# Optimization experiments

Hardware: AMD Instinct MI355X
Metric: run time of the kernel (lower is better)

Reference implementation:

```python
import jax, jax.numpy as jnp
import numpy as np

ATTN_MASK_VALUE = -1e10
N = 8192
DIM = 1024
DIM_HEAD = 64
DIM_OUT = 1024

def setup_inputs() -> dict:
    key = jax.random.key(0)
    k1, k2, k3 = jax.random.split(key, 3)
    x = jax.random.normal(k1, (N, DIM), dtype=jnp.float32)
    Wqkv = jax.random.normal(k2, (DIM, 3 * DIM_HEAD), dtype=jnp.float32) * (DIM ** -0.5)
    Wout = jax.random.normal(k3, (DIM_HEAD, DIM_OUT), dtype=jnp.float32) * (DIM_HEAD ** -0.5)
    bout = jnp.zeros((DIM_OUT,), dtype=jnp.float32)
    return {"x": x, "Wqkv": Wqkv, "Wout": Wout, "bout": bout}

def reference(x, Wqkv, Wout, bout) -> jnp.ndarray:
    n = x.shape[0]
    scale = DIM_HEAD ** -0.5
    qkv = x @ Wqkv                      # [n, 3*dh]
    q, k, v = jnp.split(qkv, 3, axis=-1)  # each [n, dh]
    sim = jnp.einsum('id,jd->ij', q, k) * scale  # [n, n]
    mask = jnp.tril(jnp.ones((n, n), dtype=bool))
    sim = jnp.where(mask, sim, ATTN_MASK_VALUE)
    attn = jax.nn.softmax(sim, axis=-1)
    out = jnp.einsum('ij,jd->id', attn, v)  # [n, dh]
    return out @ Wout + bout            # [n, dim_out]
```

## Files before the change

kernel.cpp:

```cpp
#include <hip/hip_runtime.h>
#include <hip/hip_bf16.h>

#define N_TOK 8192

typedef float f32x4  __attribute__((ext_vector_type(4)));
typedef float f32x16 __attribute__((ext_vector_type(16)));
typedef short bf16x8 __attribute__((ext_vector_type(8)));
typedef unsigned int u32x4 __attribute__((ext_vector_type(4)));

__device__ inline short f2bf(float f) {
    union { __hip_bfloat16 h; short s; } u;
    u.h = __float2bfloat16(f);
    return u.s;
}
__device__ inline unsigned cvtpk(float lo, float hi) {
    unsigned r;
    asm("v_cvt_pk_bf16_f32 %0, %1, %2" : "=v"(r) : "v"(lo), "v"(hi));
    return r;
}
__device__ inline void plswap(unsigned &a, unsigned &b) {
    asm("v_permlane32_swap_b32 %0, %1" : "+v"(a), "+v"(b));
}

#define PREC 2080


__global__ __launch_bounds__(256) void conv_kernel(
    const float* __restrict__ Wqkv,
    const float* __restrict__ Wout,
    __hip_bfloat16* __restrict__ Wt,
    __hip_bfloat16* __restrict__ WoT) {
    __shared__ float tile[32][33];
    const int t = threadIdx.x;
    const int cc = t & 31, rbase = t >> 5;
    const int b = blockIdx.x;
    if (b < 192) {
        const int r0 = (b & 31) * 32;
        const int c0 = (b >> 5) * 32;
        #pragma unroll
        for (int it = 0; it < 4; ++it) {
            const int rr = rbase + it * 8;
            tile[rr][cc] = Wqkv[(size_t)(r0 + rr) * 192 + c0 + cc];
        }
        __syncthreads();
        #pragma unroll
        for (int it = 0; it < 4; ++it) {
            const int rr = rbase + it * 8;
            Wt[(size_t)(c0 + rr) * 1024 + r0 + cc] = __float2bfloat16(tile[cc][rr]);
        }
    } else {
        const int bb = b - 192;
        const int r0 = (bb & 1) * 32;
        const int c0 = (bb >> 1) * 32;
        #pragma unroll
        for (int it = 0; it < 4; ++it) {
            const int rr = rbase + it * 8;
            tile[rr][cc] = Wout[(size_t)(r0 + rr) * 1024 + c0 + cc];
        }
        __syncthreads();
        #pragma unroll
        for (int it = 0; it < 4; ++it) {
            const int rr = rbase + it * 8;
            WoT[(size_t)(c0 + rr) * 64 + r0 + cc] = __float2bfloat16(tile[cc][rr]);
        }
    }
}

__global__ __launch_bounds__(512) void qkv_kernel(
    const float* __restrict__ x,
    const __hip_bfloat16* __restrict__ Wt,
    __hip_bfloat16* __restrict__ Qf,
    __hip_bfloat16* __restrict__ Kf,
    __hip_bfloat16* __restrict__ Vf) {
    __shared__ __hip_bfloat16 sA[2][32 * 64];
    __shared__ __hip_bfloat16 sB[2][192 * 64];
    __shared__ __hip_bfloat16 sV[64][36];
    const int tid = threadIdx.x;
    const int w = tid >> 6, lane = tid & 63;
    const int l16 = lane & 15, lq = lane >> 4;
    const int wm = w & 1, wn = w >> 1;
    const int m0 = blockIdx.x * 32;

    const int ar = tid >> 4;
    const int ac = (tid & 15) >> 1;
    const int ah = tid & 1;
    const float* agp = x + (size_t)(m0 + ar) * 1024 + ac * 8 + ah * 4;
    const int aoff = ar * 64 + ((ac ^ (ar & 7)) * 8) + ah * 4;

    int boff[3];
    const __hip_bfloat16* bgp[3];
    #pragma unroll
    for (int i = 0; i < 3; ++i) {
        const int q = i * 512 + tid;
        const int r = q >> 3, c = q & 7;
        bgp[i] = Wt + (size_t)r * 1024 + c * 8;
        boff[i] = r * 64 + ((c ^ (r & 7)) * 8);
    }

    const int arow = wm * 16 + l16;
    const int aswz0 = arow * 64 + ((lq ^ (arow & 7)) * 8);
    const int aswz1 = arow * 64 + (((4 + lq) ^ (arow & 7)) * 8);
    int bswz0[3], bswz1[3];
    #pragma unroll
    for (int j = 0; j < 3; ++j) {
        const int row = wn * 48 + j * 16 + l16;
        bswz0[j] = row * 64 + ((lq ^ (row & 7)) * 8);
        bswz1[j] = row * 64 + (((4 + lq) ^ (row & 7)) * 8);
    }

    f32x4 acc[3];
    #pragma unroll
    for (int j = 0; j < 3; ++j) acc[j] = (f32x4)0.f;

    float4 areg;
    u32x4 breg[3];

    areg = *reinterpret_cast<const float4*>(agp);
    #pragma unroll
    for (int i = 0; i < 3; ++i)
        breg[i] = *reinterpret_cast<const u32x4*>(bgp[i]);
    {
        uint2 aw; aw.x = cvtpk(areg.x, areg.y); aw.y = cvtpk(areg.z, areg.w);
        *reinterpret_cast<uint2*>(&sA[0][aoff]) = aw;
        #pragma unroll
        for (int i = 0; i < 3; ++i)
            *reinterpret_cast<u32x4*>(&sB[0][boff[i]]) = breg[i];
    }
    __syncthreads();

    for (int ks = 0; ks < 16; ++ks) {
        const int cur = ks & 1;
        if (ks < 15) {
            areg = *reinterpret_cast<const float4*>(agp + (ks + 1) * 64);
            #pragma unroll
            for (int i = 0; i < 3; ++i)
                breg[i] = *reinterpret_cast<const u32x4*>(bgp[i] + (ks + 1) * 64);
        }
        bf16x8 af0 = *reinterpret_cast<const bf16x8*>(&sA[cur][aswz0]);
        bf16x8 af1 = *reinterpret_cast<const bf16x8*>(&sA[cur][aswz1]);
        #pragma unroll
        for (int j = 0; j < 3; ++j) {
            bf16x8 b0 = *reinterpret_cast<const bf16x8*>(&sB[cur][bswz0[j]]);
            bf16x8 b1 = *reinterpret_cast<const bf16x8*>(&sB[cur][bswz1[j]]);
            acc[j] = __builtin_amdgcn_mfma_f32_16x16x32_bf16(b0, af0, acc[j], 0, 0, 0);
            acc[j] = __builtin_amdgcn_mfma_f32_16x16x32_bf16(b1, af1, acc[j], 0, 0, 0);
        }
        if (ks < 15) {
            uint2 aw; aw.x = cvtpk(areg.x, areg.y); aw.y = cvtpk(areg.z, areg.w);
            *reinterpret_cast<uint2*>(&sA[cur ^ 1][aoff]) = aw;
            #pragma unroll
            for (int i = 0; i < 3; ++i)
                *reinterpret_cast<u32x4*>(&sB[cur ^ 1][boff[i]]) = breg[i];
        }
        __syncthreads();
    }

    const int row = m0 + wm * 16 + l16;
    #pragma unroll
    for (int j = 0; j < 3; ++j) {
        const int nt = wn * 3 + j;
        const int nb = nt * 16 + 4 * lq;
        if (nt < 4) {
            const int tq = row >> 5, lr = row & 31;
            const int kc = nb >> 4, hi2 = (nb >> 3) & 1, jj = nb & 7;
            short4 qs;
            qs.x = f2bf(acc[j][0] * 0.18033688011112042f);
            qs.y = f2bf(acc[j][1] * 0.18033688011112042f);
            qs.z = f2bf(acc[j][2] * 0.18033688011112042f);
            qs.w = f2bf(acc[j][3] * 0.18033688011112042f);
            *reinterpret_cast<short4*>(Qf + ((size_t)(tq * 4 + kc) * 64 + lr + 32 * hi2) * 8 + jj) = qs;
        } else if (nt < 8) {
            const int col = nb - 64;
            const int c = row >> 6, rr = row & 63, hk = rr >> 5, lr = rr & 31;
            const int kc = col >> 4, hi2 = (col >> 3) & 1, jj = col & 7;
            short4 ks4;
            ks4.x = f2bf(acc[j][0]); ks4.y = f2bf(acc[j][1]);
            ks4.z = f2bf(acc[j][2]); ks4.w = f2bf(acc[j][3]);
            *reinterpret_cast<short4*>(Kf + ((size_t)(c * 8 + 4 * hk + kc) * 64 + lr + 32 * hi2) * 8 + jj) = ks4;
        } else {
            #pragma unroll
            for (int r = 0; r < 4; ++r)
                sV[nb + r - 128][wm * 16 + l16] = __float2bfloat16(acc[j][r]);
        }
    }
    __syncthreads();
    const int vd = tid >> 3, vm = (tid & 7) * 4;
    short4 vv = *reinterpret_cast<const short4*>(&sV[vd][vm]);
    const int kv = m0 + vm;
    const int c = kv >> 6, ks2 = (kv >> 4) & 3, hi2 = (kv >> 3) & 1, jj = kv & 7;
    *reinterpret_cast<short4*>(Vf + ((size_t)(c * 8 + 4 * (vd >> 5) + ks2) * 64 + (vd & 31) + 32 * hi2) * 8 + jj) = vv;
}

__global__ __launch_bounds__(512) void attn_kernel(
    const __hip_bfloat16* __restrict__ Qf,
    const __hip_bfloat16* __restrict__ Kf,
    const __hip_bfloat16* __restrict__ Vf,
    float* __restrict__ Part) {
    __shared__ float sO[8][64][32];
    __shared__ float sL[8][32];
    const int tid = threadIdx.x;
    const int w = tid >> 6, lane = tid & 63;
    const int l31 = lane & 31, hi = lane >> 5;
    const int p = blockIdx.x >> 2, s = blockIdx.x & 3;
    const int slot = w * 4 + s;

    for (int ti = 0; ti < 2; ++ti) {
        const int t = ti ? (255 - p) : p;
        const int q0 = t * 32;
        const int Ct = (q0 + 95) >> 6;
        const int qabs = q0 + l31;

        bf16x8 qf[4];
        #pragma unroll
        for (int kc = 0; kc < 4; ++kc)
            qf[kc] = *reinterpret_cast<const bf16x8*>(
                Qf + ((size_t)(t * 4 + kc) * 64 + lane) * 8);

        float l = 0.f;
        f32x16 Oa = (f32x16)0.f, Oc = (f32x16)0.f;

        if (slot < Ct) {
            bf16x8 ka[4], kb2[4], va[4], vb[4];
            {
                const __hip_bfloat16* kp = Kf + (size_t)slot * 4096 + lane * 8;
                const __hip_bfloat16* vp = Vf + (size_t)slot * 4096 + lane * 8;
                #pragma unroll
                for (int kc = 0; kc < 4; ++kc) {
                    ka[kc]  = *reinterpret_cast<const bf16x8*>(kp + kc * 512);
                    kb2[kc] = *reinterpret_cast<const bf16x8*>(kp + 2048 + kc * 512);
                    va[kc]  = *reinterpret_cast<const bf16x8*>(vp + kc * 512);
                    vb[kc]  = *reinterpret_cast<const bf16x8*>(vp + 2048 + kc * 512);
                }
            }

            for (int c = slot; c < Ct; c += 32) {
                const int kv0 = c * 64;
                const bool more = (c + 32) < Ct;

                f32x16 Sa = (f32x16)(-16.f), Sb = (f32x16)(-16.f);
                #pragma unroll
                for (int kc = 0; kc < 4; ++kc)
                    Sa = __builtin_amdgcn_mfma_f32_32x32x16_bf16(ka[kc], qf[kc], Sa, 0, 0, 0);
                #pragma unroll
                for (int kc = 0; kc < 4; ++kc)
                    Sb = __builtin_amdgcn_mfma_f32_32x32x16_bf16(kb2[kc], qf[kc], Sb, 0, 0, 0);

                if (more) {
                    const __hip_bfloat16* kn = Kf + (size_t)(c + 32) * 4096 + lane * 8;
                    #pragma unroll
                    for (int kc = 0; kc < 4; ++kc) {
                        ka[kc]  = *reinterpret_cast<const bf16x8*>(kn + kc * 512);
                        kb2[kc] = *reinterpret_cast<const bf16x8*>(kn + 2048 + kc * 512);
                    }
                }

                if (kv0 + 64 > q0) {
                    #pragma unroll
                    for (int r = 0; r < 16; ++r) {
                        const int rowk = (r & 3) + 8 * (r >> 2) + 4 * hi;
                        if (kv0 + rowk > qabs)      Sa[r] = -1.0e30f;
                        if (kv0 + 32 + rowk > qabs) Sb[r] = -1.0e30f;
                    }
                }

                #pragma unroll
                for (int r = 0; r < 16; ++r) Sa[r] = exp2f(Sa[r]);
                #pragma unroll
                for (int r = 0; r < 16; ++r) Sb[r] = exp2f(Sb[r]);
                float s8[8];
                #pragma unroll
                for (int j = 0; j < 8; ++j)
                    s8[j] = (Sa[2*j] + Sa[2*j+1]) + (Sb[2*j] + Sb[2*j+1]);
                #pragma unroll
                for (int j = 0; j < 4; ++j) s8[j] += s8[j+4];
                float ps = (s8[0] + s8[2]) + (s8[1] + s8[3]);
                ps += __shfl_xor(ps, 32);
                l += ps;

                bf16x8 F0, F1, F2, F3;
                {
                    unsigned a0 = cvtpk(Sa[0], Sa[1]),  a1 = cvtpk(Sa[2], Sa[3]);
                    unsigned a2 = cvtpk(Sa[4], Sa[5]),  a3 = cvtpk(Sa[6], Sa[7]);
                    plswap(a0, a2); plswap(a1, a3);
                    u32x4 w0; w0[0]=a0; w0[1]=a1; w0[2]=a2; w0[3]=a3;
                    F0 = __builtin_bit_cast(bf16x8, w0);
                    unsigned b0 = cvtpk(Sa[8], Sa[9]),  b1 = cvtpk(Sa[10], Sa[11]);
                    unsigned b2 = cvtpk(Sa[12], Sa[13]), b3 = cvtpk(Sa[14], Sa[15]);
                    plswap(b0, b2); plswap(b1, b3);
                    u32x4 w1; w1[0]=b0; w1[1]=b1; w1[2]=b2; w1[3]=b3;
                    F1 = __builtin_bit_cast(bf16x8, w1);
                    unsigned c0_ = cvtpk(Sb[0], Sb[1]),  c1_ = cvtpk(Sb[2], Sb[3]);
                    unsigned c2_ = cvtpk(Sb[4], Sb[5]),  c3_ = cvtpk(Sb[6], Sb[7]);
                    plswap(c0_, c2_); plswap(c1_, c3_);
                    u32x4 w2; w2[0]=c0_; w2[1]=c1_; w2[2]=c2_; w2[3]=c3_;
                    F2 = __builtin_bit_cast(bf16x8, w2);
                    unsigned d0 = cvtpk(Sb[8], Sb[9]),  d1 = cvtpk(Sb[10], Sb[11]);
                    unsigned d2 = cvtpk(Sb[12], Sb[13]), d3 = cvtpk(Sb[14], Sb[15]);
                    plswap(d0, d2); plswap(d1, d3);
                    u32x4 w3; w3[0]=d0; w3[1]=d1; w3[2]=d2; w3[3]=d3;
                    F3 = __builtin_bit_cast(bf16x8, w3);
                }
                bf16x8 Fa[4] = {F0, F1, F2, F3};
                #pragma unroll
                for (int ks = 0; ks < 4; ++ks) {
                    Oa = __builtin_amdgcn_mfma_f32_32x32x16_bf16(va[ks], Fa[ks], Oa, 0, 0, 0);
                    Oc = __builtin_amdgcn_mfma_f32_32x32x16_bf16(vb[ks], Fa[ks], Oc, 0, 0, 0);
                }

                if (more) {
                    const __hip_bfloat16* vn = Vf + (size_t)(c + 32) * 4096 + lane * 8;
                    #pragma unroll
                    for (int ks = 0; ks < 4; ++ks) {
                        va[ks] = *reinterpret_cast<const bf16x8*>(vn + ks * 512);
                        vb[ks] = *reinterpret_cast<const bf16x8*>(vn + 2048 + ks * 512);
                    }
                }
            }
        }

        if (hi == 0) sL[w][l31] = l;
        #pragma unroll
        for (int r = 0; r < 16; ++r) {
            const int d = (r & 3) + 8 * (r >> 2) + 4 * hi;
            sO[w][d][l31]      = Oa[r];
            sO[w][d + 32][l31] = Oc[r];
        }
        __syncthreads();

        float* pb = Part + (size_t)(t * 4 + s) * PREC;
        for (int e = tid; e < 2048; e += 512) {
            const int d = e >> 5, qq = e & 31;
            float ob = 0.f;
            #pragma unroll
            for (int wi = 0; wi < 8; ++wi) ob += sO[wi][d][qq];
            pb[e] = ob;
            if (d == 0) {
                float lb = 0.f;
                #pragma unroll
                for (int wi = 0; wi < 8; ++wi) lb += sL[wi][qq];
                pb[2048 + qq] = lb;
            }
        }
        __syncthreads();
    }
}

__global__ __launch_bounds__(256) void merge_kernel(
    const float* __restrict__ Part, __hip_bfloat16* __restrict__ Ob) {
    const int t = blockIdx.x, q0 = t * 32;
    const float* pp = Part + (size_t)(t * 4) * PREC;
    for (int e = threadIdx.x; e < 2048; e += 256) {
        const int qq = e & 31, d = e >> 5;
        float ll = 0.f, oo = 0.f;
        #pragma unroll
        for (int si = 0; si < 4; ++si) {
            ll += pp[si * PREC + 2048 + qq];
            oo += pp[si * PREC + d * 32 + qq];
        }
        Ob[(size_t)(q0 + qq) * 64 + d] = __float2bfloat16(oo / ll);
    }
}

__global__ __launch_bounds__(256) void out_kernel(
    const __hip_bfloat16* __restrict__ Ob,
    const __hip_bfloat16* __restrict__ WoT,
    const float* __restrict__ bout,
    float* __restrict__ out) {
    const int tid = threadIdx.x;
    const int w = tid >> 6, lane = tid & 63;
    const int l16 = lane & 15, lq = lane >> 4;
    const int m0 = blockIdx.x * 64 + w * 16;
    const int n0 = blockIdx.y * 256;

    const __hip_bfloat16* orow = Ob + (size_t)(m0 + l16) * 64;
    bf16x8 a0 = *reinterpret_cast<const bf16x8*>(orow + 8 * lq);
    bf16x8 a1 = *reinterpret_cast<const bf16x8*>(orow + 32 + 8 * lq);

    const int row = m0 + l16;
    for (int nt = 0; nt < 16; ++nt) {
        const __hip_bfloat16* wrow = WoT + (size_t)(n0 + nt * 16 + l16) * 64;
        bf16x8 b0 = *reinterpret_cast<const bf16x8*>(wrow + 8 * lq);
        bf16x8 b1 = *reinterpret_cast<const bf16x8*>(wrow + 32 + 8 * lq);
        f32x4 acc = (f32x4)0.f;
        acc = __builtin_amdgcn_mfma_f32_16x16x32_bf16(b0, a0, acc, 0, 0, 0);
        acc = __builtin_amdgcn_mfma_f32_16x16x32_bf16(b1, a1, acc, 0, 0, 0);
        const int nb = n0 + nt * 16 + 4 * lq;
        float4 bb = *reinterpret_cast<const float4*>(bout + nb);
        float4 res;
        res.x = acc[0] + bb.x; res.y = acc[1] + bb.y;
        res.z = acc[2] + bb.z; res.w = acc[3] + bb.w;
        *reinterpret_cast<float4*>(out + (size_t)row * 1024 + nb) = res;
    }
}

extern "C" void kernel_launch(void* const* d_in, const int* in_sizes, int n_in,
                              void* d_out, int out_size, void* d_ws, size_t ws_size,
                              hipStream_t stream) {
    const float* x    = (const float*)d_in[0];
    const float* Wqkv = (const float*)d_in[1];
    const float* Wout = (const float*)d_in[2];
    const float* bout = (const float*)d_in[3];
    float* out = (float*)d_out;

    char* ws = (char*)d_ws;
    __hip_bfloat16* Wt  = (__hip_bfloat16*)(ws);
    __hip_bfloat16* WoT = (__hip_bfloat16*)(ws + 393216);
    __hip_bfloat16* Qf  = (__hip_bfloat16*)(ws + 524288);
    __hip_bfloat16* Kf  = (__hip_bfloat16*)(ws + 1572864);
    __hip_bfloat16* Vf  = (__hip_bfloat16*)(ws + 2621440);
    __hip_bfloat16* Ob  = (__hip_bfloat16*)(ws + 3670016);
    float*          Part = (float*)(ws + 4718592);

    conv_kernel<<<256, 256, 0, stream>>>(Wqkv, Wout, Wt, WoT);
    qkv_kernel<<<256, 512, 0, stream>>>(x, Wt, Qf, Kf, Vf);
    attn_kernel<<<512, 512, 0, stream>>>(Qf, Kf, Vf, Part);
    merge_kernel<<<256, 256, 0, stream>>>(Part, Ob);
    out_kernel<<<dim3(128, 4), 256, 0, stream>>>(Ob, WoT, bout, out);
}
```

Measured before the change: 72.22 us.

## Share double-buffered K/V tiles in LDS across four query waves with 8-way KV split

The attention kernel now runs 4-wave blocks, where each wave owns a different 32-query tile of a 128-query block. K/V chunks are staged once per block into double-buffered LDS and shared by all four waves, instead of every wave streaming its own chunks from global memory into registers. The KV range is split 8 ways across blocks, and each wave writes its partial output and row sum directly, which removes the in-block LDS reduction. The merge kernel now sums 8 partials instead of 4. The cost is a per-iteration block barrier, more partial traffic and a larger Part buffer, and load imbalance between the causal query blocks.

```diff
diff --git a/kernel.cpp b/kernel.cpp
--- a/kernel.cpp
+++ b/kernel.cpp
@@ -191,67 +191,69 @@
     *reinterpret_cast<short4*>(Vf + ((size_t)(c * 8 + 4 * (vd >> 5) + ks2) * 64 + (vd & 31) + 32 * hi2) * 8 + jj) = vv;
 }
 
-__global__ __launch_bounds__(512) void attn_kernel(
+__global__ __launch_bounds__(256) void attn_kernel(
     const __hip_bfloat16* __restrict__ Qf,
     const __hip_bfloat16* __restrict__ Kf,
     const __hip_bfloat16* __restrict__ Vf,
     float* __restrict__ Part) {
-    __shared__ float sO[8][64][32];
-    __shared__ float sL[8][32];
+    __shared__ __hip_bfloat16 sK[2][4096];
+    __shared__ __hip_bfloat16 sV2[2][4096];
     const int tid = threadIdx.x;
     const int w = tid >> 6, lane = tid & 63;
     const int l31 = lane & 31, hi = lane >> 5;
-    const int p = blockIdx.x >> 2, s = blockIdx.x & 3;
-    const int slot = w * 4 + s;
-
-    for (int ti = 0; ti < 2; ++ti) {
-        const int t = ti ? (255 - p) : p;
-        const int q0 = t * 32;
-        const int Ct = (q0 + 95) >> 6;
-        const int qabs = q0 + l31;
-
-        bf16x8 qf[4];
-        #pragma unroll
-        for (int kc = 0; kc < 4; ++kc)
-            qf[kc] = *reinterpret_cast<const bf16x8*>(
-                Qf + ((size_t)(t * 4 + kc) * 64 + lane) * 8);
-
-        float l = 0.f;
-        f32x16 Oa = (f32x16)0.f, Oc = (f32x16)0.f;
-
-        if (slot < Ct) {
-            bf16x8 ka[4], kb2[4], va[4], vb[4];
-            {
-                const __hip_bfloat16* kp = Kf + (size_t)slot * 4096 + lane * 8;
-                const __hip_bfloat16* vp = Vf + (size_t)slot * 4096 + lane * 8;
+    const int qb = 63 - (int)(blockIdx.x >> 3);
+    const int s = blockIdx.x & 7;
+    const int tq = qb * 4 + w;
+    const int q0 = tq * 32;
+    const int CtB = 2 * qb + 2;
+    const int Ctw = (q0 + 95) >> 6;
+    const int qabs = q0 + l31;
+
+    bf16x8 qf[4];
+    #pragma unroll
+    for (int kc = 0; kc < 4; ++kc)
+        qf[kc] = *reinterpret_cast<const bf16x8*>(
+            Qf + ((size_t)(tq * 4 + kc) * 64 + lane) * 8);
+
+    float l = 0.f;
+    f32x16 Oa = (f32x16)0.f, Oc = (f32x16)0.f;
+
+    if (s < CtB) {
+        const size_t toff = (size_t)tid * 8;
+        u32x4 st0, st1, st2, st3;
+
+        st0 = *reinterpret_cast<const u32x4*>(Kf + (size_t)s * 4096 + toff);
+        st1 = *reinterpret_cast<const u32x4*>(Kf + (size_t)s * 4096 + 2048 + toff);
+        st2 = *reinterpret_cast<const u32x4*>(Vf + (size_t)s * 4096 + toff);
+        st3 = *reinterpret_cast<const u32x4*>(Vf + (size_t)s * 4096 + 2048 + toff);
+        *reinterpret_cast<u32x4*>(&sK[0][toff])          = st0;
+        *reinterpret_cast<u32x4*>(&sK[0][toff + 2048])   = st1;
+        *reinterpret_cast<u32x4*>(&sV2[0][toff])         = st2;
+        *reinterpret_cast<u32x4*>(&sV2[0][toff + 2048])  = st3;
+        __syncthreads();
+
+        int cur = 0;
+        for (int c = s; c < CtB; c += 8) {
+            const bool more = (c + 8) < CtB;
+            if (more) {
+                st0 = *reinterpret_cast<const u32x4*>(Kf + (size_t)(c + 8) * 4096 + toff);
+                st1 = *reinterpret_cast<const u32x4*>(Kf + (size_t)(c + 8) * 4096 + 2048 + toff);
+                st2 = *reinterpret_cast<const u32x4*>(Vf + (size_t)(c + 8) * 4096 + toff);
+                st3 = *reinterpret_cast<const u32x4*>(Vf + (size_t)(c + 8) * 4096 + 2048 + toff);
+            }
+
+            if (c < Ctw) {
+                const int kv0 = c * 64;
+                f32x16 Sa = (f32x16)(-16.f), Sb = (f32x16)(-16.f);
                 #pragma unroll
                 for (int kc = 0; kc < 4; ++kc) {
-                    ka[kc]  = *reinterpret_cast<const bf16x8*>(kp + kc * 512);
-                    kb2[kc] = *reinterpret_cast<const bf16x8*>(kp + 2048 + kc * 512);
-                    va[kc]  = *reinterpret_cast<const bf16x8*>(vp + kc * 512);
-                    vb[kc]  = *reinterpret_cast<const bf16x8*>(vp + 2048 + kc * 512);
+                    bf16x8 ka = *reinterpret_cast<const bf16x8*>(&sK[cur][(kc * 64 + lane) * 8]);
+                    Sa = __builtin_amdgcn_mfma_f32_32x32x16_bf16(ka, qf[kc], Sa, 0, 0, 0);
                 }
-            }
-
-            for (int c = slot; c < Ct; c += 32) {
-                const int kv0 = c * 64;
-                const bool more = (c + 32) < Ct;
-
-                f32x16 Sa = (f32x16)(-16.f), Sb = (f32x16)(-16.f);
-                #pragma unroll
-                for (int kc = 0; kc < 4; ++kc)
-                    Sa = __builtin_amdgcn_mfma_f32_32x32x16_bf16(ka[kc], qf[kc], Sa, 0, 0, 0);
-                #pragma unroll
-                for (int kc = 0; kc < 4; ++kc)
-                    Sb = __builtin_amdgcn_mfma_f32_32x32x16_bf16(kb2[kc], qf[kc], Sb, 0, 0, 0);
-
-                if (more) {
-                    const __hip_bfloat16* kn = Kf + (size_t)(c + 32) * 4096 + lane * 8;
-                    #pragma unroll
-                    for (int kc = 0; kc < 4; ++kc) {
-                        ka[kc]  = *reinterpret_cast<const bf16x8*>(kn + kc * 512);
-                        kb2[kc] = *reinterpret_cast<const bf16x8*>(kn + 2048 + kc * 512);
-                    }
+                #pragma unroll
+                for (int kc = 0; kc < 4; ++kc) {
+                    bf16x8 kb2 = *reinterpret_cast<const bf16x8*>(&sK[cur][((4 + kc) * 64 + lane) * 8]);
+                    Sb = __builtin_amdgcn_mfma_f32_32x32x16_bf16(kb2, qf[kc], Sb, 0, 0, 0);
                 }
 
                 if (kv0 + 64 > q0) {
@@ -303,57 +305,43 @@
                 bf16x8 Fa[4] = {F0, F1, F2, F3};
                 #pragma unroll
                 for (int ks = 0; ks < 4; ++ks) {
-                    Oa = __builtin_amdgcn_mfma_f32_32x32x16_bf16(va[ks], Fa[ks], Oa, 0, 0, 0);
-                    Oc = __builtin_amdgcn_mfma_f32_32x32x16_bf16(vb[ks], Fa[ks], Oc, 0, 0, 0);
-                }
-
-                if (more) {
-                    const __hip_bfloat16* vn = Vf + (size_t)(c + 32) * 4096 + lane * 8;
-                    #pragma unroll
-                    for (int ks = 0; ks < 4; ++ks) {
-                        va[ks] = *reinterpret_cast<const bf16x8*>(vn + ks * 512);
-                        vb[ks] = *reinterpret_cast<const bf16x8*>(vn + 2048 + ks * 512);
-                    }
+                    bf16x8 va = *reinterpret_cast<const bf16x8*>(&sV2[cur][(ks * 64 + lane) * 8]);
+                    bf16x8 vb = *reinterpret_cast<const bf16x8*>(&sV2[cur][((4 + ks) * 64 + lane) * 8]);
+                    Oa = __builtin_amdgcn_mfma_f32_32x32x16_bf16(va, Fa[ks], Oa, 0, 0, 0);
+                    Oc = __builtin_amdgcn_mfma_f32_32x32x16_bf16(vb, Fa[ks], Oc, 0, 0, 0);
                 }
             }
-        }
-
-        if (hi == 0) sL[w][l31] = l;
-        #pragma unroll
-        for (int r = 0; r < 16; ++r) {
-            const int d = (r & 3) + 8 * (r >> 2) + 4 * hi;
-            sO[w][d][l31]      = Oa[r];
-            sO[w][d + 32][l31] = Oc[r];
-        }
-        __syncthreads();
-
-        float* pb = Part + (size_t)(t * 4 + s) * PREC;
-        for (int e = tid; e < 2048; e += 512) {
-            const int d = e >> 5, qq = e & 31;
-            float ob = 0.f;
-            #pragma unroll
-            for (int wi = 0; wi < 8; ++wi) ob += sO[wi][d][qq];
-            pb[e] = ob;
-            if (d == 0) {
-                float lb = 0.f;
-                #pragma unroll
-                for (int wi = 0; wi < 8; ++wi) lb += sL[wi][qq];
-                pb[2048 + qq] = lb;
+
+            if (more) {
+                *reinterpret_cast<u32x4*>(&sK[cur ^ 1][toff])         = st0;
+                *reinterpret_cast<u32x4*>(&sK[cur ^ 1][toff + 2048])  = st1;
+                *reinterpret_cast<u32x4*>(&sV2[cur ^ 1][toff])        = st2;
+                *reinterpret_cast<u32x4*>(&sV2[cur ^ 1][toff + 2048]) = st3;
             }
-        }
-        __syncthreads();
-    }
+            __syncthreads();
+            cur ^= 1;
+        }
+    }
+
+    float* rec = Part + (size_t)(tq * 8 + s) * PREC;
+    #pragma unroll
+    for (int r = 0; r < 16; ++r) {
+        const int d = (r & 3) + 8 * (r >> 2) + 4 * hi;
+        rec[d * 32 + l31]        = Oa[r];
+        rec[(d + 32) * 32 + l31] = Oc[r];
+    }
+    if (hi == 0) rec[2048 + l31] = l;
 }
 
 __global__ __launch_bounds__(256) void merge_kernel(
     const float* __restrict__ Part, __hip_bfloat16* __restrict__ Ob) {
     const int t = blockIdx.x, q0 = t * 32;
-    const float* pp = Part + (size_t)(t * 4) * PREC;
+    const float* pp = Part + (size_t)(t * 8) * PREC;
     for (int e = threadIdx.x; e < 2048; e += 256) {
         const int qq = e & 31, d = e >> 5;
         float ll = 0.f, oo = 0.f;
         #pragma unroll
-        for (int si = 0; si < 4; ++si) {
+        for (int si = 0; si < 8; ++si) {
             ll += pp[si * PREC + 2048 + qq];
             oo += pp[si * PREC + d * 32 + qq];
         }
@@ -413,7 +401,7 @@
 
     conv_kernel<<<256, 256, 0, stream>>>(Wqkv, Wout, Wt, WoT);
     qkv_kernel<<<256, 512, 0, stream>>>(x, Wt, Qf, Kf, Vf);
-    attn_kernel<<<512, 512, 0, stream>>>(Qf, Kf, Vf, Part);
+    attn_kernel<<<512, 256, 0, stream>>>(Qf, Kf, Vf, Part);
     merge_kernel<<<256, 256, 0, stream>>>(Part, Ob);
     out_kernel<<<dim3(128, 4), 256, 0, stream>>>(Ob, WoT, bout, out);
 }
```

Result: slower. 77.54 us (+7.4%).
